# Kernel optimization log

Measured on AMD Instinct MI355X. Metric: run time of the kernel, lower is better.

Reference implementation:

```python
import jax, jax.numpy as jnp
import numpy as np

ALPHA = 0.2  # LeakyReLU negative slope

def setup_inputs() -> dict:
    key = jax.random.key(0)
    k1, k2, k3, k4, k5, k6, k7 = jax.random.split(key, 7)
    N, E, IN, OUT, R = 50000, 800000, 64, 64, 200
    inp = {
        'input': jax.random.normal(k1, (N, IN), dtype=jnp.float32),
        'edge': jax.random.randint(k2, (2, E), 0, N, dtype=jnp.int64),
        'edge_embed': jax.random.normal(k3, (E, 64), dtype=jnp.float32),
        'edge_type': jax.random.randint(k4, (E,), 0, R, dtype=jnp.int64),
        'granularity_labels': jax.random.uniform(k5, (N, R), dtype=jnp.float32),
        # learned params: a [out, 2*in], a_2 [1, out] (xavier-normal-ish)
        'a': jax.random.normal(k6, (OUT, 2 * IN), dtype=jnp.float32) * (1.414 * (2.0 / (OUT + 2 * IN)) ** 0.5),
        'a_2': jax.random.normal(k7, (1, OUT), dtype=jnp.float32) * (1.414 * (2.0 / (1 + OUT)) ** 0.5),
    }
    return inp

def reference(input, edge, edge_embed, edge_type, granularity_labels, a, a_2):
    N = input.shape[0]
    src, dst = edge[0], edge[1]
    # per-edge gather + score: edge_h [E, 2*in], edge_m [E, out]
    edge_h = jnp.concatenate([input[src], input[dst]], axis=1)
    edge_m = edge_h @ a.T
    # granularity weighting per edge
    gran = 0.5 * (granularity_labels[src, edge_type] + granularity_labels[dst, edge_type])  # [E]
    weighted_edge_m = edge_m * gran[:, None]  # [E, out]
    # scalar score per edge, exp(-leaky_relu(.)) (unnormalized attention)
    raw_e = weighted_edge_m @ a_2[0]  # [E]
    edge_e = jnp.exp(-jax.nn.leaky_relu(raw_e, ALPHA))  # [E]
    # sparse softmax denominator via segment sum over source nodes
    e_rowsum = jax.ops.segment_sum(edge_e, src, num_segments=N)  # [N]
    e_rowsum = jnp.where(e_rowsum == 0.0, 1e-12, e_rowsum)
    # SPMM aggregate (dropout=0 / eval => identity)
    edge_w = edge_e[:, None] * weighted_edge_m  # [E, out]
    h_prime = jax.ops.segment_sum(edge_w, src, num_segments=N)  # [N, out]
    h_prime = h_prime / e_rowsum[:, None]
    return jax.nn.elu(h_prime)
```

## Files before the change

### kernel.cpp

```cpp
#include <hip/hip_runtime.h>
#include <hip/hip_bf16.h>


#define LRELU_ALPHA 0.2f
#define SCAN_BLOCK 256
#define SCAN_ITEMS 8
#define SCAN_TILE (SCAN_BLOCK * SCAN_ITEMS)
#define PITCH 72

typedef __attribute__((ext_vector_type(8))) short bf16x8;
typedef __attribute__((ext_vector_type(4))) float f32x4;

__device__ __forceinline__ float bflo(unsigned int q) {
    return __int_as_float((int)(q << 16));
}
__device__ __forceinline__ float bfhi(unsigned int q) {
    return __int_as_float((int)(q & 0xffff0000u));
}
__device__ __forceinline__ unsigned short f2bf(float f) {
    __hip_bfloat16 h = __float2bfloat16(f);
    return *reinterpret_cast<unsigned short*>(&h);
}

__global__ __launch_bounds__(256) void prep_b_kernel(
    const float* __restrict__ a, unsigned short* __restrict__ Bg)
{
    const int idx = blockIdx.x * 256 + threadIdx.x;
    if (idx < 128 * 64) {
        const int op = idx >> 6, i = idx & 63;
        const float val = (op < 64) ? a[op * 128 + i] : a[(op - 64) * 128 + 64 + i];
        Bg[idx] = f2bf(val);
    }
}

__global__ __launch_bounds__(256) void node_mfma_kernel(
    const float* __restrict__ x, const unsigned short* __restrict__ Bg,
    const float* __restrict__ a2,
    unsigned short* __restrict__ u_bf, unsigned short* __restrict__ v_bf,
    float* __restrict__ su, float* __restrict__ sv,
    int* __restrict__ count, int N)
{
    __shared__ unsigned short xl[64 * PITCH];
    __shared__ unsigned short bl[128 * PITCH];
    const int t = threadIdx.x;
    const int rowbase = blockIdx.x * 64;

    {
        const int row = t & 63, q = t >> 6;
        const int grow = rowbase + row;
        float xv[16];
        if (grow < N) {
            const float4* xp = (const float4*)(x + (size_t)grow * 64 + q * 16);
#pragma unroll
            for (int k = 0; k < 4; ++k) {
                const float4 f = xp[k];
                xv[k * 4 + 0] = f.x; xv[k * 4 + 1] = f.y;
                xv[k * 4 + 2] = f.z; xv[k * 4 + 3] = f.w;
            }
        } else {
#pragma unroll
            for (int k = 0; k < 16; ++k) xv[k] = 0.f;
        }
        unsigned int uu[8];
#pragma unroll
        for (int k = 0; k < 8; ++k)
            uu[k] = (unsigned int)f2bf(xv[2 * k]) |
                    ((unsigned int)f2bf(xv[2 * k + 1]) << 16);
        uint4* dst = (uint4*)&xl[row * PITCH + q * 16];
        dst[0] = make_uint4(uu[0], uu[1], uu[2], uu[3]);
        dst[1] = make_uint4(uu[4], uu[5], uu[6], uu[7]);
    }
    {
        const int op = t >> 1, h = (t & 1) * 32;
        const uint4* src = (const uint4*)(Bg + op * 64 + h);
        uint4* dst = (uint4*)&bl[op * PITCH + h];
#pragma unroll
        for (int k = 0; k < 4; ++k) dst[k] = src[k];
    }
    if (t < 64 && rowbase + t < N) count[rowbase + t] = 0;
    __syncthreads();

    const int w = t >> 6, l = t & 63;
    const int rw = w * 16;
    const int lr = l & 15, lk = l >> 4;

    const bf16x8 af0 = *(const bf16x8*)&xl[(rw + lr) * PITCH + lk * 8];
    const bf16x8 af1 = *(const bf16x8*)&xl[(rw + lr) * PITCH + 32 + lk * 8];

    float sup[4] = {0.f, 0.f, 0.f, 0.f}, svp[4] = {0.f, 0.f, 0.f, 0.f};

    for (int ct = 0; ct < 8; ++ct) {
        const bf16x8 bf0 = *(const bf16x8*)&bl[(ct * 16 + lr) * PITCH + lk * 8];
        const bf16x8 bf1 = *(const bf16x8*)&bl[(ct * 16 + lr) * PITCH + 32 + lk * 8];
        f32x4 acc = {0.f, 0.f, 0.f, 0.f};
        acc = __builtin_amdgcn_mfma_f32_16x16x32_bf16(af0, bf0, acc, 0, 0, 0);
        acc = __builtin_amdgcn_mfma_f32_16x16x32_bf16(af1, bf1, acc, 0, 0, 0);

        const int col = ct * 16 + lr;
        unsigned short* dst = (ct < 4) ? u_bf : v_bf;
        const int o = (ct < 4) ? col : col - 64;
        const float a2o = a2[o];
#pragma unroll
        for (int r = 0; r < 4; ++r) {
            const int grow = rowbase + rw + lk * 4 + r;
            if (grow < N) dst[(size_t)grow * 64 + o] = f2bf(acc[r]);
            if (ct < 4) sup[r] += acc[r] * a2o; else svp[r] += acc[r] * a2o;
        }
    }

#pragma unroll
    for (int r = 0; r < 4; ++r) {
#pragma unroll
        for (int m = 1; m < 16; m <<= 1) {
            sup[r] += __shfl_xor(sup[r], m, 64);
            svp[r] += __shfl_xor(svp[r], m, 64);
        }
    }
    if (lr == 0) {
#pragma unroll
        for (int r = 0; r < 4; ++r) {
            const int grow = rowbase + rw + lk * 4 + r;
            if (grow < N) { su[grow] = sup[r]; sv[grow] = svp[r]; }
        }
    }
}

__global__ __launch_bounds__(256) void hist_kernel(
    const int* __restrict__ edge, int* __restrict__ count,
    int* __restrict__ rank, int E)
{
    const int i4 = (blockIdx.x * 256 + threadIdx.x) * 4;
    if (i4 + 3 < E) {
        const int4 s4 = *(const int4*)(edge + i4);
        int4 r4;
        r4.x = atomicAdd(&count[s4.x], 1);
        r4.y = atomicAdd(&count[s4.y], 1);
        r4.z = atomicAdd(&count[s4.z], 1);
        r4.w = atomicAdd(&count[s4.w], 1);
        *(int4*)(rank + i4) = r4;
    } else {
        for (int i = i4; i < E; ++i)
            rank[i] = atomicAdd(&count[edge[i]], 1);
    }
}

__global__ __launch_bounds__(256) void scan_blocks_kernel(
    const int* __restrict__ count, int* __restrict__ base,
    int* __restrict__ blocksums, int N)
{
    __shared__ int lds[SCAN_BLOCK];
    const int b = blockIdx.x, t = threadIdx.x;
    const int idx0 = b * SCAN_TILE + t * SCAN_ITEMS;
    int vals[SCAN_ITEMS];
    int s = 0;
#pragma unroll
    for (int k = 0; k < SCAN_ITEMS; ++k) {
        const int idx = idx0 + k;
        const int c = (idx < N) ? count[idx] : 0;
        vals[k] = s; s += c;
    }
    lds[t] = s;
    __syncthreads();
    for (int off = 1; off < SCAN_BLOCK; off <<= 1) {
        const int xv = (t >= off) ? lds[t - off] : 0;
        __syncthreads();
        lds[t] += xv;
        __syncthreads();
    }
    const int excl = (t == 0) ? 0 : lds[t - 1];
#pragma unroll
    for (int k = 0; k < SCAN_ITEMS; ++k) {
        const int idx = idx0 + k;
        if (idx < N) base[idx] = excl + vals[k];
    }
    if (t == SCAN_BLOCK - 1) blocksums[b] = lds[t];
}

__global__ void scan_tops_kernel(int* __restrict__ blocksums, int nb)
{
    if (threadIdx.x == 0 && blockIdx.x == 0) {
        int s = 0;
        for (int i = 0; i < nb; ++i) { const int c = blocksums[i]; blocksums[i] = s; s += c; }
    }
}

__global__ __launch_bounds__(256) void edge_place_kernel(
    const int* __restrict__ edge, const int* __restrict__ etype,
    const int* __restrict__ base, const int* __restrict__ blocksums,
    const int* __restrict__ rank,
    unsigned int* __restrict__ csr, int E, int N, int R)
{
    const int e = blockIdx.x * 256 + threadIdx.x;
    if (e >= E) return;
    const int s = edge[e];
    const int d = edge[(size_t)E + e];
    const int t = etype[e];
    if ((unsigned)s >= (unsigned)N || (unsigned)d >= (unsigned)N ||
        (unsigned)t >= (unsigned)R) return;

    const int pos = base[s] + blocksums[s / SCAN_TILE] + rank[e];
    csr[pos] = ((unsigned)d << 8) | (unsigned)t;
}

__global__ __launch_bounds__(256) void aggregate_kernel(
    const int* __restrict__ base, const int* __restrict__ blocksums,
    const unsigned int* __restrict__ csr,
    const uint2* __restrict__ u_bf4,
    const uint2* __restrict__ v_bf4,
    const float* __restrict__ su, const float* __restrict__ sv,
    const float* __restrict__ G, int R,
    float* __restrict__ out, int N, int E)
{
    const int wave = threadIdx.x >> 6;
    const int lane = threadIdx.x & 63;
    const int n = blockIdx.x * 4 + wave;
    if (n >= N) return;

    const int rs = base[n] + blocksums[n / SCAN_TILE];
    const int re = (n + 1 < N) ? (base[n + 1] + blocksums[(n + 1) / SCAN_TILE]) : E;

    const int c = lane & 15;
    const int r = lane >> 4;

    const float su_n = su[n];
    const float* __restrict__ Gn = G + (size_t)n * R;

    float v0 = 0.f, v1 = 0.f, v2 = 0.f, v3 = 0.f;
    float sumw_p = 0.f, sumee_p = 0.f;

    for (int i = rs; i < re; i += 64) {
        const int m = min(64, re - i);
        int dl = 0; float wl = 0.f, eel = 0.f;
        if (lane < m) {
            const unsigned p = csr[i + lane];
            const int d = (int)(p >> 8);
            const int t = (int)(p & 255u);
            const float g   = 0.5f * (Gn[t] + G[(size_t)d * R + t]);
            const float raw = g * (su_n + sv[d]);
            const float lr  = raw > 0.f ? raw : LRELU_ALPHA * raw;
            const float ee  = __expf(-lr);
            dl  = d;
            eel = ee;
            wl  = ee * g;
        }
        sumw_p  += wl;
        sumee_p += eel;
        for (int j = 0; j < m; j += 8) {
            const int   jA = j + r;
            const int   jB = j + 4 + r;
            const int   dA = __shfl(dl, jA, 64);
            const float wA = __shfl(wl, jA, 64);
            const int   dB = __shfl(dl, jB, 64);
            const float wB = __shfl(wl, jB, 64);
            const uint2 qa = v_bf4[(size_t)dA * 16 + c];
            const uint2 qb = v_bf4[(size_t)dB * 16 + c];
            v0 += wA * bflo(qa.x);
            v1 += wA * bfhi(qa.x);
            v2 += wA * bflo(qa.y);
            v3 += wA * bfhi(qa.y);
            v0 += wB * bflo(qb.x);
            v1 += wB * bfhi(qb.x);
            v2 += wB * bflo(qb.y);
            v3 += wB * bfhi(qb.y);
        }
    }

    float sumw = sumw_p, sumee = sumee_p;
#pragma unroll
    for (int m2 = 1; m2 < 64; m2 <<= 1) {
        sumw  += __shfl_xor(sumw,  m2, 64);
        sumee += __shfl_xor(sumee, m2, 64);
    }
    v0 += __shfl_xor(v0, 16, 64);  v0 += __shfl_xor(v0, 32, 64);
    v1 += __shfl_xor(v1, 16, 64);  v1 += __shfl_xor(v1, 32, 64);
    v2 += __shfl_xor(v2, 16, 64);  v2 += __shfl_xor(v2, 32, 64);
    v3 += __shfl_xor(v3, 16, 64);  v3 += __shfl_xor(v3, 32, 64);

    const uint2 qu = u_bf4[(size_t)n * 16 + c];
    v0 += sumw * bflo(qu.x);
    v1 += sumw * bfhi(qu.x);
    v2 += sumw * bflo(qu.y);
    v3 += sumw * bfhi(qu.y);

    const float rden = (sumee == 0.f) ? 1e-12f : sumee;
    const float h0 = v0 / rden, h1 = v1 / rden, h2 = v2 / rden, h3 = v3 / rden;
    if (lane < 16) {
        float4 o;
        o.x = (h0 > 0.f) ? h0 : expm1f(h0);
        o.y = (h1 > 0.f) ? h1 : expm1f(h1);
        o.z = (h2 > 0.f) ? h2 : expm1f(h2);
        o.w = (h3 > 0.f) ? h3 : expm1f(h3);
        ((float4*)out)[(size_t)n * 16 + c] = o;
    }
}

extern "C" void kernel_launch(void* const* d_in, const int* in_sizes, int n_in,
                              void* d_out, int out_size, void* d_ws, size_t ws_size,
                              hipStream_t stream)
{
    const float* x     = (const float*)d_in[0];
    const int*   edge  = (const int*)d_in[1];
    const int*   etype = (const int*)d_in[3];
    const float* G     = (const float*)d_in[4];
    const float* a     = (const float*)d_in[5];
    const float* a2    = (const float*)d_in[6];

    const int N = in_sizes[0] / 64;
    const int E = in_sizes[1] / 2;
    const int R = in_sizes[4] / N;

    float* out = (float*)d_out;

    unsigned short* u_bf = (unsigned short*)d_ws;
    unsigned short* v_bf = u_bf + (size_t)N * 64;
    float* su     = (float*)(v_bf + (size_t)N * 64);
    float* sv     = su + N;
    int*   count  = (int*)(sv + N);
    int*   base   = count + N;
    const int nsb = (N + SCAN_TILE - 1) / SCAN_TILE;
    int*   blocksums = base + N;
    int*   rank   = blocksums + ((nsb + 63) & ~63);
    unsigned int* csr = (unsigned int*)(rank + E);
    unsigned short* Bg = (unsigned short*)(csr + E);
    Bg = (unsigned short*)((((uintptr_t)Bg) + 15) & ~(uintptr_t)15);

    prep_b_kernel<<<dim3(32), dim3(256), 0, stream>>>(a, Bg);
    node_mfma_kernel<<<dim3((N + 63) / 64), dim3(256), 0, stream>>>(
        x, Bg, a2, u_bf, v_bf, su, sv, count, N);
    hist_kernel<<<dim3(((E + 3) / 4 + 255) / 256), dim3(256), 0, stream>>>(
        edge, count, rank, E);
    scan_blocks_kernel<<<dim3(nsb), dim3(SCAN_BLOCK), 0, stream>>>(count, base, blocksums, N);
    scan_tops_kernel<<<dim3(1), dim3(64), 0, stream>>>(blocksums, nsb);
    edge_place_kernel<<<dim3((E + 255) / 256), dim3(256), 0, stream>>>(
        edge, etype, base, blocksums, rank, csr, E, N, R);
    aggregate_kernel<<<dim3((N + 3) / 4), dim3(256), 0, stream>>>(
        base, blocksums, csr, (const uint2*)u_bf, (const uint2*)v_bf,
        su, sv, G, R, out, N, E);
}
```

Measured before the change: 117.7 us.

## Fold prep and scan-tops kernels into consumers, vectorize edge placement, prefetch gathers

Removes the separate bf16 weight-prep kernel by converting `a` inside the node MFMA kernel, and replaces the single-thread scan_tops kernel with a per-block wave-level prefix scan of blocksums in LDS. Edge placement now handles four edges per thread using int4 loads. In the aggregate loop, the first sixteen neighbour feature rows are loaded before the score computation so gather latency overlaps the exp math. Each block redundantly rescans up to 64 blocksums and each node block reconverts the weights, which is a small amount of extra work per block. The int4 edge loads assume the edge, etype and rank arrays are 16-byte aligned, and the LDS scan only covers nsb up to 64.

```diff
diff --git a/kernel.cpp b/kernel.cpp
--- a/kernel.cpp
+++ b/kernel.cpp
@@ -22,19 +22,8 @@
     return *reinterpret_cast<unsigned short*>(&h);
 }
 
-__global__ __launch_bounds__(256) void prep_b_kernel(
-    const float* __restrict__ a, unsigned short* __restrict__ Bg)
-{
-    const int idx = blockIdx.x * 256 + threadIdx.x;
-    if (idx < 128 * 64) {
-        const int op = idx >> 6, i = idx & 63;
-        const float val = (op < 64) ? a[op * 128 + i] : a[(op - 64) * 128 + 64 + i];
-        Bg[idx] = f2bf(val);
-    }
-}
-
 __global__ __launch_bounds__(256) void node_mfma_kernel(
-    const float* __restrict__ x, const unsigned short* __restrict__ Bg,
+    const float* __restrict__ x, const float* __restrict__ a,
     const float* __restrict__ a2,
     unsigned short* __restrict__ u_bf, unsigned short* __restrict__ v_bf,
     float* __restrict__ su, float* __restrict__ sv,
@@ -71,11 +60,18 @@
         dst[1] = make_uint4(uu[4], uu[5], uu[6], uu[7]);
     }
     {
-        const int op = t >> 1, h = (t & 1) * 32;
-        const uint4* src = (const uint4*)(Bg + op * 64 + h);
-        uint4* dst = (uint4*)&bl[op * PITCH + h];
-#pragma unroll
-        for (int k = 0; k < 4; ++k) dst[k] = src[k];
+        const int op = t >> 1, hh = (t & 1) * 32;
+        const float* src = (op < 64) ? (a + op * 128 + hh)
+                                     : (a + (op - 64) * 128 + 64 + hh);
+        unsigned int uu[16];
+#pragma unroll
+        for (int k = 0; k < 16; ++k)
+            uu[k] = (unsigned int)f2bf(src[2 * k]) |
+                    ((unsigned int)f2bf(src[2 * k + 1]) << 16);
+        uint4* dst = (uint4*)&bl[op * PITCH + hh];
+#pragma unroll
+        for (int k = 0; k < 4; ++k)
+            dst[k] = make_uint4(uu[4 * k], uu[4 * k + 1], uu[4 * k + 2], uu[4 * k + 3]);
     }
     if (t < 64 && rowbase + t < N) count[rowbase + t] = 0;
     __syncthreads();
@@ -176,34 +172,66 @@
     if (t == SCAN_BLOCK - 1) blocksums[b] = lds[t];
 }
 
-__global__ void scan_tops_kernel(int* __restrict__ blocksums, int nb)
-{
-    if (threadIdx.x == 0 && blockIdx.x == 0) {
-        int s = 0;
-        for (int i = 0; i < nb; ++i) { const int c = blocksums[i]; blocksums[i] = s; s += c; }
-    }
+__device__ __forceinline__ void scan_blocksums_lds(
+    const int* __restrict__ blocksums, int nsb, int* pfx)
+{
+    const int tid = threadIdx.x;
+    if (tid < 64) {
+        const int raw = (tid < nsb) ? blocksums[tid] : 0;
+        int bv = raw;
+#pragma unroll
+        for (int o = 1; o < 64; o <<= 1) {
+            const int xv = __shfl_up(bv, o, 64);
+            if (tid >= o) bv += xv;
+        }
+        pfx[tid] = bv - raw;
+    }
+    __syncthreads();
 }
 
 __global__ __launch_bounds__(256) void edge_place_kernel(
     const int* __restrict__ edge, const int* __restrict__ etype,
-    const int* __restrict__ base, const int* __restrict__ blocksums,
+    const int* __restrict__ base, const int* __restrict__ blocksums, int nsb,
     const int* __restrict__ rank,
     unsigned int* __restrict__ csr, int E, int N, int R)
 {
-    const int e = blockIdx.x * 256 + threadIdx.x;
-    if (e >= E) return;
-    const int s = edge[e];
-    const int d = edge[(size_t)E + e];
-    const int t = etype[e];
-    if ((unsigned)s >= (unsigned)N || (unsigned)d >= (unsigned)N ||
-        (unsigned)t >= (unsigned)R) return;
-
-    const int pos = base[s] + blocksums[s / SCAN_TILE] + rank[e];
-    csr[pos] = ((unsigned)d << 8) | (unsigned)t;
+    __shared__ int pfx[64];
+    scan_blocksums_lds(blocksums, nsb, pfx);
+
+    const int i4 = (blockIdx.x * 256 + threadIdx.x) * 4;
+    if (i4 + 3 < E) {
+        const int4 s4 = *(const int4*)(edge + i4);
+        const int4 d4 = *(const int4*)(edge + (size_t)E + i4);
+        const int4 t4 = *(const int4*)(etype + i4);
+        const int4 r4 = *(const int4*)(rank + i4);
+        const int ss[4] = {s4.x, s4.y, s4.z, s4.w};
+        const int dd[4] = {d4.x, d4.y, d4.z, d4.w};
+        const int tt[4] = {t4.x, t4.y, t4.z, t4.w};
+        const int rr[4] = {r4.x, r4.y, r4.z, r4.w};
+#pragma unroll
+        for (int k = 0; k < 4; ++k) {
+            if ((unsigned)ss[k] < (unsigned)N && (unsigned)dd[k] < (unsigned)N &&
+                (unsigned)tt[k] < (unsigned)R) {
+                const int pos = base[ss[k]] + pfx[ss[k] / SCAN_TILE] + rr[k];
+                csr[pos] = ((unsigned)dd[k] << 8) | (unsigned)tt[k];
+            }
+        }
+    } else {
+        for (int i = i4; i < E; ++i) {
+            const int s = edge[i];
+            const int d = edge[(size_t)E + i];
+            const int t = etype[i];
+            if ((unsigned)s < (unsigned)N && (unsigned)d < (unsigned)N &&
+                (unsigned)t < (unsigned)R) {
+                const int pos = base[s] + pfx[s / SCAN_TILE] + rank[i];
+                csr[pos] = ((unsigned)d << 8) | (unsigned)t;
+            }
+        }
+    }
 }
 
 __global__ __launch_bounds__(256) void aggregate_kernel(
-    const int* __restrict__ base, const int* __restrict__ blocksums,
+    const int* __restrict__ base, const int* __restrict__ blocksums, int nsb,
     const unsigned int* __restrict__ csr,
     const uint2* __restrict__ u_bf4,
     const uint2* __restrict__ v_bf4,
@@ -211,13 +239,16 @@
     const float* __restrict__ G, int R,
     float* __restrict__ out, int N, int E)
 {
+    __shared__ int pfx[64];
+    scan_blocksums_lds(blocksums, nsb, pfx);
+
     const int wave = threadIdx.x >> 6;
     const int lane = threadIdx.x & 63;
     const int n = blockIdx.x * 4 + wave;
     if (n >= N) return;
 
-    const int rs = base[n] + blocksums[n / SCAN_TILE];
-    const int re = (n + 1 < N) ? (base[n + 1] + blocksums[(n + 1) / SCAN_TILE]) : E;
+    const int rs = base[n] + pfx[n / SCAN_TILE];
+    const int re = (n + 1 < N) ? (base[n + 1] + pfx[(n + 1) / SCAN_TILE]) : E;
 
     const int c = lane & 15;
     const int r = lane >> 4;
@@ -230,22 +261,52 @@
 
     for (int i = rs; i < re; i += 64) {
         const int m = min(64, re - i);
-        int dl = 0; float wl = 0.f, eel = 0.f;
+        unsigned pe = 0;
+        if (lane < m) pe = csr[i + lane];
+        const int dl = (int)(pe >> 8);
+
+        const int   dA0 = __shfl(dl, 0 + r, 64);
+        const int   dB0 = __shfl(dl, 4 + r, 64);
+        const uint2 qa0 = v_bf4[(size_t)dA0 * 16 + c];
+        const uint2 qb0 = v_bf4[(size_t)dB0 * 16 + c];
+        uint2 qa1 = make_uint2(0u, 0u), qb1 = make_uint2(0u, 0u);
+        if (m > 8) {
+            const int dA1 = __shfl(dl, 8 + r, 64);
+            const int dB1 = __shfl(dl, 12 + r, 64);
+            qa1 = v_bf4[(size_t)dA1 * 16 + c];
+            qb1 = v_bf4[(size_t)dB1 * 16 + c];
+        }
+
+        float wl = 0.f, eel = 0.f;
         if (lane < m) {
-            const unsigned p = csr[i + lane];
-            const int d = (int)(p >> 8);
-            const int t = (int)(p & 255u);
-            const float g   = 0.5f * (Gn[t] + G[(size_t)d * R + t]);
-            const float raw = g * (su_n + sv[d]);
+            const int t = (int)(pe & 255u);
+            const float g   = 0.5f * (Gn[t] + G[(size_t)dl * R + t]);
+            const float raw = g * (su_n + sv[dl]);
             const float lr  = raw > 0.f ? raw : LRELU_ALPHA * raw;
             const float ee  = __expf(-lr);
-            dl  = d;
             eel = ee;
             wl  = ee * g;
         }
         sumw_p  += wl;
         sumee_p += eel;
-        for (int j = 0; j < m; j += 8) {
+
+        {
+            const float wA = __shfl(wl, 0 + r, 64);
+            const float wB = __shfl(wl, 4 + r, 64);
+            v0 += wA * bflo(qa0.x);  v1 += wA * bfhi(qa0.x);
+            v2 += wA * bflo(qa0.y);  v3 += wA * bfhi(qa0.y);
+            v0 += wB * bflo(qb0.x);  v1 += wB * bfhi(qb0.x);
+            v2 += wB * bflo(qb0.y);  v3 += wB * bfhi(qb0.y);
+        }
+        if (m > 8) {
+            const float wA = __shfl(wl, 8 + r, 64);
+            const float wB = __shfl(wl, 12 + r, 64);
+            v0 += wA * bflo(qa1.x);  v1 += wA * bfhi(qa1.x);
+            v2 += wA * bflo(qa1.y);  v3 += wA * bfhi(qa1.y);
+            v0 += wB * bflo(qb1.x);  v1 += wB * bfhi(qb1.x);
+            v2 += wB * bflo(qb1.y);  v3 += wB * bfhi(qb1.y);
+        }
+        for (int j = 16; j < m; j += 8) {
             const int   jA = j + r;
             const int   jB = j + 4 + r;
             const int   dA = __shfl(dl, jA, 64);
@@ -254,14 +315,10 @@
             const float wB = __shfl(wl, jB, 64);
             const uint2 qa = v_bf4[(size_t)dA * 16 + c];
             const uint2 qb = v_bf4[(size_t)dB * 16 + c];
-            v0 += wA * bflo(qa.x);
-            v1 += wA * bfhi(qa.x);
-            v2 += wA * bflo(qa.y);
-            v3 += wA * bfhi(qa.y);
-            v0 += wB * bflo(qb.x);
-            v1 += wB * bfhi(qb.x);
-            v2 += wB * bflo(qb.y);
-            v3 += wB * bfhi(qb.y);
+            v0 += wA * bflo(qa.x);  v1 += wA * bfhi(qa.x);
+            v2 += wA * bflo(qa.y);  v3 += wA * bfhi(qa.y);
+            v0 += wB * bflo(qb.x);  v1 += wB * bfhi(qb.x);
+            v2 += wB * bflo(qb.y);  v3 += wB * bfhi(qb.y);
         }
     }
 
@@ -321,19 +378,15 @@
     int*   blocksums = base + N;
     int*   rank   = blocksums + ((nsb + 63) & ~63);
     unsigned int* csr = (unsigned int*)(rank + E);
-    unsigned short* Bg = (unsigned short*)(csr + E);
-    Bg = (unsigned short*)((((uintptr_t)Bg) + 15) & ~(uintptr_t)15);
-
-    prep_b_kernel<<<dim3(32), dim3(256), 0, stream>>>(a, Bg);
+
     node_mfma_kernel<<<dim3((N + 63) / 64), dim3(256), 0, stream>>>(
-        x, Bg, a2, u_bf, v_bf, su, sv, count, N);
+        x, a, a2, u_bf, v_bf, su, sv, count, N);
     hist_kernel<<<dim3(((E + 3) / 4 + 255) / 256), dim3(256), 0, stream>>>(
         edge, count, rank, E);
     scan_blocks_kernel<<<dim3(nsb), dim3(SCAN_BLOCK), 0, stream>>>(count, base, blocksums, N);
-    scan_tops_kernel<<<dim3(1), dim3(64), 0, stream>>>(blocksums, nsb);
-    edge_place_kernel<<<dim3((E + 255) / 256), dim3(256), 0, stream>>>(
-        edge, etype, base, blocksums, rank, csr, E, N, R);
+    edge_place_kernel<<<dim3(((E + 3) / 4 + 255) / 256), dim3(256), 0, stream>>>(
+        edge, etype, base, blocksums, nsb, rank, csr, E, N, R);
     aggregate_kernel<<<dim3((N + 3) / 4), dim3(256), 0, stream>>>(
-        base, blocksums, csr, (const uint2*)u_bf, (const uint2*)v_bf,
+        base, blocksums, nsb, csr, (const uint2*)u_bf, (const uint2*)v_bf,
         su, sv, G, R, out, N, E);
 }
```

New measurement: 111.6 us. 1.06x faster.
